# Optimization experiments

Measured on AMD Instinct MI355X. Metric: run time of the kernel, lower is better.

The kernel has to match this reference:

```python
import jax, jax.numpy as jnp
import numpy as np

K_SIZE, STRIDE, PAD = 3, 1, 1
B, C1, C2, H, W = 2, 256, 256, 64, 64


def conv2d(x, w, b, stride, pad):
    out = jax.lax.conv_general_dilated(
        x, w, (stride, stride), [(pad, pad), (pad, pad)],
        dimension_numbers=("NCHW", "OIHW", "NCHW"))
    return out + b[None, :, None, None]


def deform_conv2d(x, offset, mask, w, b, k, stride, pad):
    # torchvision.ops.deform_conv2d semantics (modulated, offset_groups=1)
    Bn, C, Hh, Ww = x.shape
    Ho, Wo = offset.shape[2], offset.shape[3]
    K = k * k
    # offset channels are (dy, dx) interleaved per kernel point
    off = offset.reshape(Bn, K, 2, Ho, Wo)
    dy, dx = off[:, :, 0], off[:, :, 1]          # [B,K,Ho,Wo]
    ki = jnp.arange(k)
    kyy, kxx = jnp.meshgrid(ki, ki, indexing="ij")
    kyy, kxx = kyy.reshape(K), kxx.reshape(K)
    base_y = (jnp.arange(Ho) * stride - pad)[None, :, None] + kyy[:, None, None]  # [K,Ho,1]
    base_x = (jnp.arange(Wo) * stride - pad)[None, None, :] + kxx[:, None, None]  # [K,1,Wo]
    ys = base_y[None].astype(x.dtype) + dy       # [B,K,Ho,Wo]
    xs = base_x[None].astype(x.dtype) + dx
    N = K * Ho * Wo
    ysf, xsf = ys.reshape(Bn, N), xs.reshape(Bn, N)
    y0 = jnp.floor(ysf)
    x0 = jnp.floor(xsf)
    ly, lx = ysf - y0, xsf - x0                  # bilinear fractions
    y0i, x0i = y0.astype(jnp.int32), x0.astype(jnp.int32)
    xf = x.reshape(Bn, C, Hh * Ww)

    def gather(yi, xi):
        valid = (yi >= 0) & (yi < Hh) & (xi >= 0) & (xi < Ww)
        idx = jnp.clip(yi, 0, Hh - 1) * Ww + jnp.clip(xi, 0, Ww - 1)
        v = jnp.take_along_axis(xf, idx[:, None, :], axis=2)  # [B,C,N]
        return v * valid[:, None, :].astype(x.dtype)

    v00 = gather(y0i, x0i)
    v01 = gather(y0i, x0i + 1)
    v10 = gather(y0i + 1, x0i)
    v11 = gather(y0i + 1, x0i + 1)
    wy1, wx1 = ly[:, None], lx[:, None]
    val = (v00 * (1 - wy1) * (1 - wx1) + v01 * (1 - wy1) * wx1 +
           v10 * wy1 * (1 - wx1) + v11 * wy1 * wx1)          # [B,C,N]
    val = val.reshape(Bn, C, K, Ho, Wo) * mask[:, None]       # modulate
    out = jnp.einsum("ock,bckhw->bohw", w.reshape(w.shape[0], C, K), val)
    return out + b[None, :, None, None]


def setup_inputs() -> dict:
    key = jax.random.key(0)
    ks = jax.random.split(key, 6)
    k2 = K_SIZE * K_SIZE
    return {
        "x": jax.random.normal(ks[0], (B, C1, H, W), jnp.float32),
        "offset_feat": jax.random.normal(ks[1], (B, C2, H, W), jnp.float32),
        # offset/mask head conv (zero-init in module; small random so offsets are non-trivial)
        "w_offset_mask": jax.random.normal(ks[2], (3 * k2, C2, K_SIZE, K_SIZE), jnp.float32) * 0.01,
        "b_offset_mask": jax.random.normal(ks[3], (3 * k2,), jnp.float32) * 0.01,
        "w_dcn": jax.random.normal(ks[4], (C2, C1, K_SIZE, K_SIZE), jnp.float32) / np.sqrt(C1 * k2),
        "b_dcn": jax.random.normal(ks[5], (C2,), jnp.float32) * 0.01,
    }


def reference(x, offset_feat, w_offset_mask, b_offset_mask, w_dcn, b_dcn):
    om = conv2d(offset_feat, w_offset_mask, b_offset_mask, STRIDE, PAD)  # [B,3*k*k,Ho,Wo]
    o1, o2, m = jnp.split(om, 3, axis=1)
    offset = jnp.concatenate([o1, o2], axis=1)   # [B,2*k*k,Ho,Wo]
    mask = jax.nn.sigmoid(m)                      # [B,k*k,Ho,Wo]
    return deform_conv2d(x, offset, mask, w_dcn, b_dcn, K_SIZE, STRIDE, PAD)
```

## Files before the change

### kernel.cpp

```cpp
#include <hip/hip_runtime.h>
#include <math.h>

#define BATCH 2
#define CIN   256
#define COUT  256
#define COFF  256
#define HWPIX 4096
#define CKTOT 2304
#define VSTR  40
#define PH    66
#define PHW   4356
#define NKG   12

typedef __attribute__((ext_vector_type(8))) short short8;
typedef __attribute__((ext_vector_type(8))) unsigned short ushort8;
typedef __attribute__((ext_vector_type(4))) float float4v;

__device__ __forceinline__ unsigned short f2bf(float f) {
    unsigned u = __float_as_uint(f);
    unsigned r = (u + 0x7FFFu + ((u >> 16) & 1u)) >> 16;
    return (unsigned short)r;
}
__device__ __forceinline__ float bf2f(unsigned short h) {
    return __uint_as_float(((unsigned)h) << 16);
}

__global__ __launch_bounds__(256) void prep_kernel(
    const float* __restrict__ x, const float* __restrict__ feat,
    const float* __restrict__ wdcn, const float* __restrict__ wom,
    unsigned short* __restrict__ xTh,
    unsigned short* __restrict__ fh,
    unsigned short* __restrict__ whi,
    unsigned short* __restrict__ wohi,
    float* __restrict__ out)
{
    const int bid = blockIdx.x;
    const int tid = threadIdx.x;

    if (bid < 4096) {
        const bool isx = bid < 2048;
        const int lb = isx ? bid : bid - 2048;
        const int b  = lb >> 10;
        const int r  = lb & 1023;
        const int pt = r >> 3;
        const int ct = r & 7;
        __shared__ float t[32][33];
        const int tx = tid & 31, ty = tid >> 5;
        const float* src = isx ? x : feat;
        const float* sb = src + ((size_t)b * 256 + ct * 32) * HWPIX + pt * 32;
#pragma unroll
        for (int i = ty; i < 32; i += 8)
            t[i][tx] = sb[(size_t)i * HWPIX + tx];
        __syncthreads();
        if (isx) {
            unsigned short* ob = xTh + ((size_t)b * HWPIX + pt * 32) * 256 + ct * 32;
#pragma unroll
            for (int i = ty; i < 32; i += 8)
                ob[(size_t)i * 256 + tx] = f2bf(t[tx][i]);
        } else {
#pragma unroll
            for (int i = ty; i < 32; i += 8) {
                int p = pt * 32 + i;
                int row = (p >> 6) + 1, col = (p & 63) + 1;
                fh[((size_t)b * PHW + row * PH + col) * 256 + ct * 32 + tx]
                    = f2bf(t[tx][i]);
            }
        }
    } else if (bid < 6400) {
        int gid = (bid - 4096) * 256 + tid;
        int cc  = gid & 31;
        int co  = (gid >> 5) & 255;
        int kcb = gid >> 13;
        int k   = kcb >> 3;
        int cb  = kcb & 7;
        float w = wdcn[((size_t)co * 256 + cb * 32 + cc) * 9 + k];
        whi[gid] = f2bf(w);
    } else if (bid < 6688) {
        int gid = (bid - 6400) * 256 + tid;
        int cc  = gid & 31;
        int co  = (gid >> 5) & 31;
        int kcb = gid >> 10;
        int k   = kcb >> 3;
        int cb  = kcb & 7;
        float w = 0.0f;
        if (co < 27) w = wom[(size_t)co * CKTOT + (cb * 32 + cc) * 9 + k];
        wohi[gid] = f2bf(w);
    } else if (bid < 7208) {
        int idx = (bid - 6688) * 256 + tid;
        int b = idx / 66560;
        int r = idx - b * 66560;
        int pidx = r >> 8;
        int c = r & 255;
        int row, col;
        if (pidx < 66)       { row = 0;           col = pidx; }
        else if (pidx < 132) { row = 65;          col = pidx - 66; }
        else if (pidx < 196) { row = pidx - 131;  col = 0; }
        else                 { row = pidx - 195;  col = 65; }
        fh[((size_t)b * PHW + row * PH + col) * 256 + c] = 0;
    } else {
        int idx = (bid - 7208) * 256 + tid;
        ((float4*)out)[idx] = make_float4(0.f, 0.f, 0.f, 0.f);
    }
}

__global__ __launch_bounds__(256) void conv_om_mfma_kernel(
    const unsigned short* __restrict__ fh,
    const unsigned short* __restrict__ wohi,
    float* __restrict__ om12)
{
    const int y  = blockIdx.x;
    const int kg = blockIdx.y;
    const int b  = blockIdx.z;
    const int tid = threadIdx.x;
    const int wv  = tid >> 6;
    const int lane = tid & 63;
    const int l15 = lane & 15;
    const int q   = lane >> 4;
    const int xg  = wv * 16 + l15;

    float4v acc[2];
    acc[0] = (float4v)0.0f;
    acc[1] = (float4v)0.0f;

    const unsigned short* fhb = fh + (size_t)b * PHW * 256;

#pragma unroll 3
    for (int i = 0; i < 6; ++i) {
        int kcb = kg * 6 + i;
        int k  = kcb >> 3;
        int cb = kcb & 7;
        size_t s = ((size_t)((y + k / 3) * PH + xg + k % 3)) * 256 + cb * 32 + q * 8;
        short8 bh = *(const short8*)(fhb + s);
        short8 ah0 = *(const short8*)(wohi + ((size_t)kcb * 32 + l15) * 32 + q * 8);
        short8 ah1 = *(const short8*)(wohi + ((size_t)kcb * 32 + 16 + l15) * 32 + q * 8);
        acc[0] = __builtin_amdgcn_mfma_f32_16x16x32_bf16(ah0, bh, acc[0], 0, 0, 0);
        acc[1] = __builtin_amdgcn_mfma_f32_16x16x32_bf16(ah1, bh, acc[1], 0, 0, 0);
    }

    const int p = y * 64 + xg;
    float* ob = om12 + (size_t)(kg * 2 + b) * 27 * HWPIX;
#pragma unroll
    for (int t = 0; t < 2; ++t) {
#pragma unroll
        for (int r = 0; r < 4; ++r) {
            int co = t * 16 + q * 4 + r;
            if (co < 27) ob[co * HWPIX + p] = acc[t][r];
        }
    }
}

__global__ __launch_bounds__(256, 4) void dcn_mfma_kernel(
    const unsigned short* __restrict__ xTh,
    const float* __restrict__ om12,
    const unsigned short* __restrict__ whi,
    const float* __restrict__ bom,
    const float* __restrict__ bdcn,
    float* __restrict__ out)
{
    const int tid = threadIdx.x;
    const int y   = blockIdx.x >> 1;
    const int xh  = blockIdx.x & 1;
    const int cog = blockIdx.y >> 1;
    const int kg  = blockIdx.y & 1;
    const int b   = blockIdx.z;

    __shared__ float4 s_wt[288];
    __shared__ int4   s_ix[288];
    __shared__ unsigned short V[288 * VSTR];

    for (int idx = tid; idx < 288; idx += 256) {
        int k   = idx >> 5;
        int pxl = idx & 31;
        int xg  = xh * 32 + pxl;
        int p   = y * 64 + xg;
        float dy = bom[2 * k], dx = bom[2 * k + 1], mm = bom[18 + k];
#pragma unroll
        for (int g = 0; g < NKG; ++g) {
            const float* ob = om12 + (size_t)(g * 2 + b) * 27 * HWPIX;
            dy += ob[(2 * k) * HWPIX + p];
            dx += ob[(2 * k + 1) * HWPIX + p];
            mm += ob[(18 + k) * HWPIX + p];
        }
        float ys = (float)(y  - 1 + (k / 3)) + dy;
        float xs = (float)(xg - 1 + (k % 3)) + dx;
        float y0f = floorf(ys), x0f = floorf(xs);
        int y0 = (int)y0f, x0 = (int)x0f;
        float ly = ys - y0f, lx = xs - x0f;
        float m  = 1.0f / (1.0f + expf(-mm));
        bool yv0 = ((unsigned)y0 < 64u), yv1 = ((unsigned)(y0 + 1) < 64u);
        bool xv0 = ((unsigned)x0 < 64u), xv1 = ((unsigned)(x0 + 1) < 64u);
        int i00 = y0 * 64 + x0;
        float4 wt;
        int4 ix;
        wt.x = (yv0 && xv0) ? (1.0f - ly) * (1.0f - lx) * m : 0.0f;
        wt.y = (yv0 && xv1) ? (1.0f - ly) * lx * m          : 0.0f;
        wt.z = (yv1 && xv0) ? ly * (1.0f - lx) * m          : 0.0f;
        wt.w = (yv1 && xv1) ? ly * lx * m                   : 0.0f;
        ix.x = (yv0 && xv0) ? i00      : 0;
        ix.y = (yv0 && xv1) ? i00 + 1  : 0;
        ix.z = (yv1 && xv0) ? i00 + 64 : 0;
        ix.w = (yv1 && xv1) ? i00 + 65 : 0;
        s_wt[idx] = wt;
        s_ix[idx] = ix;
    }
    __syncthreads();

    const int w    = tid >> 6;
    const int lane = tid & 63;
    const int l15  = lane & 15;
    const int q    = lane >> 4;

    const int cg   = tid & 3;
    const int spx  = (tid >> 2) & 31;
    const int tapg = tid >> 7;

    float4v acc[2][2];
#pragma unroll
    for (int t = 0; t < 2; ++t)
#pragma unroll
        for (int p = 0; p < 2; ++p) acc[t][p] = (float4v)0.0f;

    const unsigned short* xb = xTh + ((size_t)b << 12) * 256;

    for (int cbl = 0; cbl < 4; ++cbl) {
        const int cb = kg * 4 + cbl;

        {
            const unsigned short* xc = xb + cb * 32 + cg * 8;
#pragma unroll 3
            for (int j = 0; j < 5; ++j) {
                int k = 2 * j + tapg;
                if (k > 8) break;
                int cidx = k * 32 + spx;
                float4 wt = s_wt[cidx];
                int4   ix = s_ix[cidx];
                ushort8 u00 = *(const ushort8*)(xc + (size_t)ix.x * 256);
                ushort8 u01 = *(const ushort8*)(xc + (size_t)ix.y * 256);
                ushort8 u10 = *(const ushort8*)(xc + (size_t)ix.z * 256);
                ushort8 u11 = *(const ushort8*)(xc + (size_t)ix.w * 256);
                unsigned hv[4];
#pragma unroll
                for (int jj = 0; jj < 4; ++jj) {
                    float va = wt.x * bf2f(u00[2 * jj])     + wt.y * bf2f(u01[2 * jj])
                             + wt.z * bf2f(u10[2 * jj])     + wt.w * bf2f(u11[2 * jj]);
                    float vb = wt.x * bf2f(u00[2 * jj + 1]) + wt.y * bf2f(u01[2 * jj + 1])
                             + wt.z * bf2f(u10[2 * jj + 1]) + wt.w * bf2f(u11[2 * jj + 1]);
                    hv[jj] = (unsigned)f2bf(va) | ((unsigned)f2bf(vb) << 16);
                }
                *(uint4*)&V[cidx * VSTR + cg * 8]
                    = make_uint4(hv[0], hv[1], hv[2], hv[3]);
            }
        }
        __syncthreads();

#pragma unroll 3
        for (int k = 0; k < 9; ++k) {
            const int kcb = k * 8 + cb;
            size_t base = ((size_t)kcb * 256 + cog * 128 + w * 32 + l15) * 32 + q * 8;
            short8 ah0 = *(const short8*)(whi + base);
            short8 ah1 = *(const short8*)(whi + base + 16 * 32);
            short8 bh0 = *(const short8*)&V[(k * 32 + l15) * VSTR + q * 8];
            short8 bh1 = *(const short8*)&V[(k * 32 + 16 + l15) * VSTR + q * 8];
            acc[0][0] = __builtin_amdgcn_mfma_f32_16x16x32_bf16(ah0, bh0, acc[0][0], 0, 0, 0);
            acc[0][1] = __builtin_amdgcn_mfma_f32_16x16x32_bf16(ah0, bh1, acc[0][1], 0, 0, 0);
            acc[1][0] = __builtin_amdgcn_mfma_f32_16x16x32_bf16(ah1, bh0, acc[1][0], 0, 0, 0);
            acc[1][1] = __builtin_amdgcn_mfma_f32_16x16x32_bf16(ah1, bh1, acc[1][1], 0, 0, 0);
        }
        __syncthreads();
    }

#pragma unroll
    for (int t = 0; t < 2; ++t) {
#pragma unroll
        for (int r = 0; r < 4; ++r) {
            int co = cog * 128 + w * 32 + t * 16 + q * 4 + r;
            float bias = (kg == 0) ? bdcn[co] : 0.0f;
#pragma unroll
            for (int p = 0; p < 2; ++p) {
                int px = xh * 32 + p * 16 + l15;
                atomicAdd(&out[(((size_t)b * COUT + co) << 12) + y * 64 + px],
                          acc[t][p][r] + bias);
            }
        }
    }
}

extern "C" void kernel_launch(void* const* d_in, const int* in_sizes, int n_in,
                              void* d_out, int out_size, void* d_ws, size_t ws_size,
                              hipStream_t stream)
{
    const float* x    = (const float*)d_in[0];
    const float* feat = (const float*)d_in[1];
    const float* wom  = (const float*)d_in[2];
    const float* bom  = (const float*)d_in[3];
    const float* wdcn = (const float*)d_in[4];
    const float* bdcn = (const float*)d_in[5];
    float* out = (float*)d_out;

    float* om12          = (float*)d_ws;
    unsigned short* whi  = (unsigned short*)(om12 + (size_t)NKG * 2 * 27 * HWPIX);
    unsigned short* wohi = whi + (size_t)CKTOT * 256;
    unsigned short* xTh  = wohi + 73728;
    unsigned short* fh   = xTh + (size_t)2 * HWPIX * 256;

    prep_kernel<<<9256, 256, 0, stream>>>(x, feat, wdcn, wom, xTh, fh,
                                          whi, wohi, out);

    dim3 gco(64, NKG, 2);
    conv_om_mfma_kernel<<<gco, 256, 0, stream>>>(fh, wohi, om12);

    dim3 grid(128, 4, 2);
    dcn_mfma_kernel<<<grid, 256, 0, stream>>>(xTh, om12, whi, bom, bdcn, out);
}
```

Baseline: 131.5 us.

## Precompute bilinear weights in a separate kernel and widen DCN blocks to all output channels

The offset/mask reduction and bilinear weight/index computation move into a new finalize kernel that writes per-pixel weight and index tables, with indices pre-scaled by the channel stride. The DCN kernel now uses 512-thread blocks that cover all 256 output channels, so each sampled V tile is built once per block instead of once per output-channel half. This removes the duplicated gathers and duplicated offset reductions, at the cost of an extra launch, an extra global round trip for the tables, and larger blocks with possibly lower occupancy.

```diff
diff --git a/kernel.cpp b/kernel.cpp
--- a/kernel.cpp
+++ b/kernel.cpp
@@ -149,59 +149,75 @@
     }
 }
 
-__global__ __launch_bounds__(256, 4) void dcn_mfma_kernel(
+__global__ __launch_bounds__(256) void finalize_om_kernel(
+    const float* __restrict__ om12,
+    const float* __restrict__ bom,
+    float4* __restrict__ wt4,
+    int4*   __restrict__ ix4)
+{
+    const int gid = blockIdx.x * 256 + threadIdx.x;
+    const int p  = gid & 4095;
+    const int bk = gid >> 12;
+    const int b  = bk / 9;
+    const int k  = bk - b * 9;
+
+    float dy = bom[2 * k], dx = bom[2 * k + 1], mm = bom[18 + k];
+#pragma unroll
+    for (int g = 0; g < NKG; ++g) {
+        const float* ob = om12 + (size_t)(g * 2 + b) * 27 * HWPIX;
+        dy += ob[(2 * k) * HWPIX + p];
+        dx += ob[(2 * k + 1) * HWPIX + p];
+        mm += ob[(18 + k) * HWPIX + p];
+    }
+    const int yy = p >> 6, xx = p & 63;
+    float ys = (float)(yy - 1 + (k / 3)) + dy;
+    float xs = (float)(xx - 1 + (k % 3)) + dx;
+    float y0f = floorf(ys), x0f = floorf(xs);
+    int y0 = (int)y0f, x0 = (int)x0f;
+    float ly = ys - y0f, lx = xs - x0f;
+    float m  = 1.0f / (1.0f + expf(-mm));
+    bool yv0 = ((unsigned)y0 < 64u), yv1 = ((unsigned)(y0 + 1) < 64u);
+    bool xv0 = ((unsigned)x0 < 64u), xv1 = ((unsigned)(x0 + 1) < 64u);
+    int i00 = (y0 * 64 + x0) << 8;
+    float4 wt;
+    int4 ix;
+    wt.x = (yv0 && xv0) ? (1.0f - ly) * (1.0f - lx) * m : 0.0f;
+    wt.y = (yv0 && xv1) ? (1.0f - ly) * lx * m          : 0.0f;
+    wt.z = (yv1 && xv0) ? ly * (1.0f - lx) * m          : 0.0f;
+    wt.w = (yv1 && xv1) ? ly * lx * m                   : 0.0f;
+    ix.x = (yv0 && xv0) ? i00          : 0;
+    ix.y = (yv0 && xv1) ? i00 + 256    : 0;
+    ix.z = (yv1 && xv0) ? i00 + 16384  : 0;
+    ix.w = (yv1 && xv1) ? i00 + 16640  : 0;
+    wt4[gid] = wt;
+    ix4[gid] = ix;
+}
+
+__global__ __launch_bounds__(512, 4) void dcn_mfma_kernel(
     const unsigned short* __restrict__ xTh,
-    const float* __restrict__ om12,
+    const float4* __restrict__ wt4,
+    const int4* __restrict__ ix4,
     const unsigned short* __restrict__ whi,
-    const float* __restrict__ bom,
     const float* __restrict__ bdcn,
     float* __restrict__ out)
 {
     const int tid = threadIdx.x;
     const int y   = blockIdx.x >> 1;
     const int xh  = blockIdx.x & 1;
-    const int cog = blockIdx.y >> 1;
-    const int kg  = blockIdx.y & 1;
+    const int kg  = blockIdx.y;
     const int b   = blockIdx.z;
 
     __shared__ float4 s_wt[288];
     __shared__ int4   s_ix[288];
     __shared__ unsigned short V[288 * VSTR];
 
-    for (int idx = tid; idx < 288; idx += 256) {
-        int k   = idx >> 5;
-        int pxl = idx & 31;
-        int xg  = xh * 32 + pxl;
-        int p   = y * 64 + xg;
-        float dy = bom[2 * k], dx = bom[2 * k + 1], mm = bom[18 + k];
-#pragma unroll
-        for (int g = 0; g < NKG; ++g) {
-            const float* ob = om12 + (size_t)(g * 2 + b) * 27 * HWPIX;
-            dy += ob[(2 * k) * HWPIX + p];
-            dx += ob[(2 * k + 1) * HWPIX + p];
-            mm += ob[(18 + k) * HWPIX + p];
-        }
-        float ys = (float)(y  - 1 + (k / 3)) + dy;
-        float xs = (float)(xg - 1 + (k % 3)) + dx;
-        float y0f = floorf(ys), x0f = floorf(xs);
-        int y0 = (int)y0f, x0 = (int)x0f;
-        float ly = ys - y0f, lx = xs - x0f;
-        float m  = 1.0f / (1.0f + expf(-mm));
-        bool yv0 = ((unsigned)y0 < 64u), yv1 = ((unsigned)(y0 + 1) < 64u);
-        bool xv0 = ((unsigned)x0 < 64u), xv1 = ((unsigned)(x0 + 1) < 64u);
-        int i00 = y0 * 64 + x0;
-        float4 wt;
-        int4 ix;
-        wt.x = (yv0 && xv0) ? (1.0f - ly) * (1.0f - lx) * m : 0.0f;
-        wt.y = (yv0 && xv1) ? (1.0f - ly) * lx * m          : 0.0f;
-        wt.z = (yv1 && xv0) ? ly * (1.0f - lx) * m          : 0.0f;
-        wt.w = (yv1 && xv1) ? ly * lx * m                   : 0.0f;
-        ix.x = (yv0 && xv0) ? i00      : 0;
-        ix.y = (yv0 && xv1) ? i00 + 1  : 0;
-        ix.z = (yv1 && xv0) ? i00 + 64 : 0;
-        ix.w = (yv1 && xv1) ? i00 + 65 : 0;
-        s_wt[idx] = wt;
-        s_ix[idx] = ix;
+    if (tid < 288) {
+        int k   = tid >> 5;
+        int pxl = tid & 31;
+        int p   = y * 64 + xh * 32 + pxl;
+        int src = ((b * 9 + k) << 12) + p;
+        s_wt[tid] = wt4[src];
+        s_ix[tid] = ix4[src];
     }
     __syncthreads();
 
@@ -228,16 +244,16 @@
         {
             const unsigned short* xc = xb + cb * 32 + cg * 8;
 #pragma unroll 3
-            for (int j = 0; j < 5; ++j) {
-                int k = 2 * j + tapg;
+            for (int j = 0; j < 3; ++j) {
+                int k = tapg + 4 * j;
                 if (k > 8) break;
                 int cidx = k * 32 + spx;
                 float4 wt = s_wt[cidx];
                 int4   ix = s_ix[cidx];
-                ushort8 u00 = *(const ushort8*)(xc + (size_t)ix.x * 256);
-                ushort8 u01 = *(const ushort8*)(xc + (size_t)ix.y * 256);
-                ushort8 u10 = *(const ushort8*)(xc + (size_t)ix.z * 256);
-                ushort8 u11 = *(const ushort8*)(xc + (size_t)ix.w * 256);
+                ushort8 u00 = *(const ushort8*)(xc + ix.x);
+                ushort8 u01 = *(const ushort8*)(xc + ix.y);
+                ushort8 u10 = *(const ushort8*)(xc + ix.z);
+                ushort8 u11 = *(const ushort8*)(xc + ix.w);
                 unsigned hv[4];
 #pragma unroll
                 for (int jj = 0; jj < 4; ++jj) {
@@ -256,7 +272,7 @@
 #pragma unroll 3
         for (int k = 0; k < 9; ++k) {
             const int kcb = k * 8 + cb;
-            size_t base = ((size_t)kcb * 256 + cog * 128 + w * 32 + l15) * 32 + q * 8;
+            size_t base = ((size_t)kcb * 256 + w * 32 + l15) * 32 + q * 8;
             short8 ah0 = *(const short8*)(whi + base);
             short8 ah1 = *(const short8*)(whi + base + 16 * 32);
             short8 bh0 = *(const short8*)&V[(k * 32 + l15) * VSTR + q * 8];
@@ -273,7 +289,7 @@
     for (int t = 0; t < 2; ++t) {
 #pragma unroll
         for (int r = 0; r < 4; ++r) {
-            int co = cog * 128 + w * 32 + t * 16 + q * 4 + r;
+            int co = w * 32 + t * 16 + q * 4 + r;
             float bias = (kg == 0) ? bdcn[co] : 0.0f;
 #pragma unroll
             for (int p = 0; p < 2; ++p) {
@@ -302,6 +318,8 @@
     unsigned short* wohi = whi + (size_t)CKTOT * 256;
     unsigned short* xTh  = wohi + 73728;
     unsigned short* fh   = xTh + (size_t)2 * HWPIX * 256;
+    float4* wt4          = (float4*)(fh + (size_t)2 * PHW * 256);
+    int4*   ix4          = (int4*)(wt4 + (size_t)2 * 9 * HWPIX);
 
     prep_kernel<<<9256, 256, 0, stream>>>(x, feat, wdcn, wom, xTh, fh,
                                           whi, wohi, out);
@@ -309,6 +327,8 @@
     dim3 gco(64, NKG, 2);
     conv_om_mfma_kernel<<<gco, 256, 0, stream>>>(fh, wohi, om12);
 
-    dim3 grid(128, 4, 2);
-    dcn_mfma_kernel<<<grid, 256, 0, stream>>>(xTh, om12, whi, bom, bdcn, out);
-}
+    finalize_om_kernel<<<288, 256, 0, stream>>>(om12, bom, wt4, ix4);
+
+    dim3 grid(128, 2, 2);
+    dcn_mfma_kernel<<<grid, 512, 0, stream>>>(xTh, wt4, ix4, whi, bdcn, out);
+}
```

Measured after the change: 131.4 us. No clear change (-0.1%).
